# Optimization experiments

Hardware: AMD Instinct MI355X
Metric: run time of the kernel (lower is better)

The kernel has to match this reference:

```python
import jax, jax.numpy as jnp
import numpy as np

N = 262144       # number of samples
DIM = 64         # feature dim
NCLASSES = 128   # number of gaussian classes


def setup_inputs() -> dict:
    key = jax.random.key(0)
    k1, k2, k3, k4 = jax.random.split(key, 4)
    inputs = jax.random.normal(k1, (N, DIM), dtype=jnp.float32)
    target = jax.random.randint(k2, (N,), 0, NCLASSES)
    mean_param = jax.random.normal(k3, (NCLASSES, DIM), dtype=jnp.float32) * 0.02
    cov_param = jax.random.normal(k4, (NCLASSES, DIM, DIM), dtype=jnp.float32) * 0.02
    return {"inputs": inputs, "target": target,
            "mean_param": mean_param, "cov_param": cov_param}


def _l2_distance(sample_mean, sample_cov_sq, mean_param, cov_param):
    # Concrete stand-in for the user-supplied `distance` callable:
    # squared-L2 between the empirical class mean and the learned means,
    # plus the energy of the empirical covariance vector and learned covariances.
    return (jnp.sum((sample_mean[None, :] - mean_param) ** 2)
            + sample_cov_sq
            + jnp.sum(cov_param ** 2))


def reference(inputs, target, mean_param, cov_param):
    nclasses = mean_param.shape[0]
    n = inputs.shape[0]
    # per-class counts and means (fused segmented reduction, one pass)
    counts = jax.ops.segment_sum(jnp.ones((n,), inputs.dtype), target,
                                 num_segments=nclasses)           # [C]
    sums = jax.ops.segment_sum(inputs, target, num_segments=nclasses)  # [C, D]
    means = sums / counts[:, None]                                 # [C, D]
    # center each sample by its class mean  (torch: temp = x - mean)
    temp = inputs - means[target]                                  # [N, D]
    # torch: cov = mm(temp, temp.T).mean(0); row k equals temp_k . mean_j(temp_j)
    # so we only need the per-class sum of centered rows (analytically ~0).
    s = jax.ops.segment_sum(temp, target, num_segments=nclasses)   # [C, D]
    cov = jnp.sum(temp * s[target], axis=-1) / counts[target]      # [N] per-sample entry
    # loss in the python loop is overwritten each iter -> only last class survives
    last = nclasses - 1
    cov_sq_last = jax.ops.segment_sum(cov * cov, target, num_segments=nclasses)[last]
    loss = _l2_distance(means[last], cov_sq_last, mean_param, cov_param)
    return loss
```

## Files before the change

### kernel.cpp

```cpp
#include <hip/hip_runtime.h>


#define DIM 64
#define NCLASSES 128
#define LAST (NCLASSES - 1)
#define NBLOCKS 128
#define BLOCK 512
#define NWAVES (NBLOCKS * 8)
#define SLOT 68
#define COLBASE (NBLOCKS * SLOT)
#define MP_PER_THREAD ((NCLASSES * DIM) / BLOCK)

__global__ __launch_bounds__(BLOCK) void gem_part(
    const float* __restrict__ inputs, const int* __restrict__ target,
    const float* __restrict__ mean_param, const float* __restrict__ cov_param,
    int n, int cov_n4, float* __restrict__ ws)
{
    const int tid  = threadIdx.x;
    const int lane = tid & 63;
    const int wib  = tid >> 6;
    const int b    = blockIdx.x;
    const int gwave = b * 8 + wib;

    const float4* c4 = (const float4*)cov_param;
    const int ci = b * BLOCK + tid;
    float4 v0 = {0.f, 0.f, 0.f, 0.f}, v1 = {0.f, 0.f, 0.f, 0.f};
    if (ci < cov_n4)                  v0 = c4[ci];
    if (ci + NBLOCKS * BLOCK < cov_n4) v1 = c4[ci + NBLOCKS * BLOCK];

    float mp[MP_PER_THREAD];
    if (b == 0) {
        #pragma unroll
        for (int k = 0; k < MP_PER_THREAD; ++k)
            mp[k] = mean_param[tid + k * BLOCK];
    }

    float acc = 0.f;
    int   cnt = 0;
    for (int base = gwave * 256; base < n; base += NWAVES * 256) {
        const int4 t4 = *(const int4*)(target + base + lane * 4);
        unsigned long long m0 = __ballot(t4.x == LAST);
        unsigned long long m1 = __ballot(t4.y == LAST);
        unsigned long long m2 = __ballot(t4.z == LAST);
        unsigned long long m3 = __ballot(t4.w == LAST);
        cnt += __popcll(m0) + __popcll(m1) + __popcll(m2) + __popcll(m3);
        #pragma unroll
        for (int j = 0; j < 4; ++j) {
            unsigned long long m = (j == 0) ? m0 : (j == 1) ? m1 : (j == 2) ? m2 : m3;
            while (m) {
                int bit = __ffsll(m) - 1;
                m &= m - 1;
                acc += inputs[(size_t)(base + 4 * bit + j) * DIM + lane];
            }
        }
    }

    float csum = v0.x * v0.x + v0.y * v0.y + v0.z * v0.z + v0.w * v0.w
               + v1.x * v1.x + v1.y * v1.y + v1.z * v1.z + v1.w * v1.w;
    for (int off = 32; off; off >>= 1) csum += __shfl_down(csum, off, 64);

    float pcol = 0.f, psq = 0.f;
    if (b == 0) {
        #pragma unroll
        for (int k = 0; k < MP_PER_THREAD; ++k) {
            pcol += mp[k];
            psq  += mp[k] * mp[k];
        }
    }
    for (int off = 32; off; off >>= 1) psq += __shfl_down(psq, off, 64);

    __shared__ float sacc[8][DIM];
    __shared__ float scol[8][DIM];
    __shared__ float scov[8], spsq[8];
    __shared__ int   scnt[8];
    sacc[wib][lane] = acc;
    scol[wib][lane] = pcol;
    if (lane == 0) { scov[wib] = csum; scnt[wib] = cnt; spsq[wib] = psq; }
    __syncthreads();

    if (wib == 0) {
        float s = 0.f;
        #pragma unroll
        for (int w = 0; w < 8; ++w) s += sacc[w][lane];
        ws[b * SLOT + lane] = s;
        if (b == 0) {
            float cs = 0.f;
            #pragma unroll
            for (int w = 0; w < 8; ++w) cs += scol[w][lane];
            ws[COLBASE + lane] = cs;
        }
    }
    if (tid == 0) {
        int   c  = 0;   float cv = 0.f, q = 0.f;
        #pragma unroll
        for (int w = 0; w < 8; ++w) { c += scnt[w]; cv += scov[w]; q += spsq[w]; }
        *(float2*)(ws + b * SLOT + DIM) = make_float2((float)c, cv);
        if (b == 0) ws[COLBASE + DIM] = q;
    }
}

__global__ __launch_bounds__(BLOCK) void gem_final(
    const float* __restrict__ ws, float* __restrict__ out)
{
    const int tid  = threadIdx.x;
    const int lane = tid & 63;
    const int g    = tid >> 6;

    const float col = (tid < DIM)  ? ws[COLBASE + tid] : 0.f;
    const float psq = (tid == 0)   ? ws[COLBASE + DIM] : 0.f;

    float s = 0.f;
    #pragma unroll
    for (int j = 0; j < NBLOCKS / 8; ++j)
        s += ws[(g + 8 * j) * SLOT + lane];

    float c = 0.f, cv = 0.f;
    if (tid < NBLOCKS) {
        float2 p = *(const float2*)(ws + tid * SLOT + DIM);
        c = p.x; cv = p.y;
    }
    for (int off = 32; off; off >>= 1) {
        c  += __shfl_down(c,  off, 64);
        cv += __shfl_down(cv, off, 64);
    }

    __shared__ float red[8][DIM];
    __shared__ float scc[2][2];
    __shared__ float spq;
    red[g][lane] = s;
    if (tid < NBLOCKS && lane == 0) { scc[g][0] = c; scc[g][1] = cv; }
    if (tid == 0) spq = psq;
    __syncthreads();

    if (tid < DIM) {
        float tot = 0.f;
        #pragma unroll
        for (int w = 0; w < 8; ++w) tot += red[w][tid];
        const float count = scc[0][0] + scc[1][0];
        const float covs  = scc[0][1] + scc[1][1];
        const float mean  = tot / count;
        float d = (float)NCLASSES * mean * mean - 2.f * mean * col;
        for (int off = 32; off; off >>= 1) d += __shfl_down(d, off, 64);
        if (tid == 0) out[0] = d + covs + spq;
    }
}

extern "C" void kernel_launch(void* const* d_in, const int* in_sizes, int n_in,
                              void* d_out, int out_size, void* d_ws, size_t ws_size,
                              hipStream_t stream) {
    const float* inputs     = (const float*)d_in[0];
    const int*   target     = (const int*)d_in[1];
    const float* mean_param = (const float*)d_in[2];
    const float* cov_param  = (const float*)d_in[3];
    float* out = (float*)d_out;
    float* ws  = (float*)d_ws;

    const int n     = in_sizes[0] / DIM;
    const int cov_n = in_sizes[3];

    gem_part<<<NBLOCKS, BLOCK, 0, stream>>>(inputs, target, mean_param, cov_param,
                                            n, cov_n / 4, ws);
    gem_final<<<1, BLOCK, 0, stream>>>(ws, out);
}
```

Measured before the change: 96.49 us.

## Compact matching sample indices in LDS and balance row gathers across waves

Each block now processes a 2048-sample chunk, compacts the indices of last-class samples into shared memory with a ballot-based prefix scan, and then splits the row gathers evenly across its 8 waves, four independent loads per iteration. Before, each wave serially walked its own ballot mask, so the load was uneven and each row load depended on the previous bit scan. In exchange the loop adds three block-wide barriers per chunk, which may cost more than the imbalance it removes given that only about 1/128 of samples match.

New measurement: 94.61 us. No clear change (-1.9%).

```diff
diff --git a/kernel.cpp b/kernel.cpp
--- a/kernel.cpp
+++ b/kernel.cpp
@@ -7,6 +7,7 @@
 #define NBLOCKS 128
 #define BLOCK 512
 #define NWAVES (NBLOCKS * 8)
+#define CHUNK (BLOCK * 4)
 #define SLOT 68
 #define COLBASE (NBLOCKS * SLOT)
 #define MP_PER_THREAD ((NCLASSES * DIM) / BLOCK)
@@ -20,12 +21,11 @@
     const int lane = tid & 63;
     const int wib  = tid >> 6;
     const int b    = blockIdx.x;
-    const int gwave = b * 8 + wib;
 
     const float4* c4 = (const float4*)cov_param;
     const int ci = b * BLOCK + tid;
     float4 v0 = {0.f, 0.f, 0.f, 0.f}, v1 = {0.f, 0.f, 0.f, 0.f};
-    if (ci < cov_n4)                  v0 = c4[ci];
+    if (ci < cov_n4)                   v0 = c4[ci];
     if (ci + NBLOCKS * BLOCK < cov_n4) v1 = c4[ci + NBLOCKS * BLOCK];
 
     float mp[MP_PER_THREAD];
@@ -35,24 +35,59 @@
             mp[k] = mean_param[tid + k * BLOCK];
     }
 
+    __shared__ int sidx[CHUNK];
+    __shared__ int swcnt[8];
     float acc = 0.f;
-    int   cnt = 0;
-    for (int base = gwave * 256; base < n; base += NWAVES * 256) {
-        const int4 t4 = *(const int4*)(target + base + lane * 4);
-        unsigned long long m0 = __ballot(t4.x == LAST);
-        unsigned long long m1 = __ballot(t4.y == LAST);
-        unsigned long long m2 = __ballot(t4.z == LAST);
-        unsigned long long m3 = __ballot(t4.w == LAST);
-        cnt += __popcll(m0) + __popcll(m1) + __popcll(m2) + __popcll(m3);
+    int   cnt_acc = 0;
+
+    for (int cbase = b * CHUNK; cbase < n; cbase += NBLOCKS * CHUNK) {
+        const int sbase = cbase + wib * 256 + lane * 4;
+        const int4 t4 = *(const int4*)(target + sbase);
+        const unsigned long long m0 = __ballot(t4.x == LAST);
+        const unsigned long long m1 = __ballot(t4.y == LAST);
+        const unsigned long long m2 = __ballot(t4.z == LAST);
+        const unsigned long long m3 = __ballot(t4.w == LAST);
+        const int c0 = __popcll(m0), c1 = __popcll(m1),
+                  c2 = __popcll(m2), c3 = __popcll(m3);
+        if (lane == 0) swcnt[wib] = c0 + c1 + c2 + c3;
+        __syncthreads();
+
+        int woff = 0, tot = 0;
         #pragma unroll
-        for (int j = 0; j < 4; ++j) {
-            unsigned long long m = (j == 0) ? m0 : (j == 1) ? m1 : (j == 2) ? m2 : m3;
-            while (m) {
-                int bit = __ffsll(m) - 1;
-                m &= m - 1;
-                acc += inputs[(size_t)(base + 4 * bit + j) * DIM + lane];
-            }
+        for (int w = 0; w < 8; ++w) {
+            int c = swcnt[w];
+            if (w < wib) woff += c;
+            tot += c;
         }
+
+        const unsigned long long lt = (1ULL << lane) - 1ULL;
+        const int r0 = __popcll(m0 & lt);
+        const int r1 = c0 + __popcll(m1 & lt);
+        const int r2 = c0 + c1 + __popcll(m2 & lt);
+        const int r3 = c0 + c1 + c2 + __popcll(m3 & lt);
+        if (t4.x == LAST) sidx[woff + r0] = sbase + 0;
+        if (t4.y == LAST) sidx[woff + r1] = sbase + 1;
+        if (t4.z == LAST) sidx[woff + r2] = sbase + 2;
+        if (t4.w == LAST) sidx[woff + r3] = sbase + 3;
+        __syncthreads();
+
+        for (int i = wib; i < tot; i += 32) {
+            const int j1 = i + 8, j2 = i + 16, j3 = i + 24;
+            const int s0 = sidx[i];
+            const int s1 = sidx[j1 < tot ? j1 : tot - 1];
+            const int s2 = sidx[j2 < tot ? j2 : tot - 1];
+            const int s3 = sidx[j3 < tot ? j3 : tot - 1];
+            const float x0 = inputs[(size_t)s0 * DIM + lane];
+            const float x1 = inputs[(size_t)s1 * DIM + lane];
+            const float x2 = inputs[(size_t)s2 * DIM + lane];
+            const float x3 = inputs[(size_t)s3 * DIM + lane];
+            acc += x0;
+            if (j1 < tot) acc += x1;
+            if (j2 < tot) acc += x2;
+            if (j3 < tot) acc += x3;
+        }
+        cnt_acc += tot;
+        __syncthreads();
     }
 
     float csum = v0.x * v0.x + v0.y * v0.y + v0.z * v0.z + v0.w * v0.w
@@ -72,10 +107,9 @@
     __shared__ float sacc[8][DIM];
     __shared__ float scol[8][DIM];
     __shared__ float scov[8], spsq[8];
-    __shared__ int   scnt[8];
     sacc[wib][lane] = acc;
     scol[wib][lane] = pcol;
-    if (lane == 0) { scov[wib] = csum; scnt[wib] = cnt; spsq[wib] = psq; }
+    if (lane == 0) { scov[wib] = csum; spsq[wib] = psq; }
     __syncthreads();
 
     if (wib == 0) {
@@ -91,10 +125,10 @@
         }
     }
     if (tid == 0) {
-        int   c  = 0;   float cv = 0.f, q = 0.f;
+        float cv = 0.f, q = 0.f;
         #pragma unroll
-        for (int w = 0; w < 8; ++w) { c += scnt[w]; cv += scov[w]; q += spsq[w]; }
-        *(float2*)(ws + b * SLOT + DIM) = make_float2((float)c, cv);
+        for (int w = 0; w < 8; ++w) { cv += scov[w]; q += spsq[w]; }
+        *(float2*)(ws + b * SLOT + DIM) = make_float2((float)cnt_acc, cv);
         if (b == 0) ws[COLBASE + DIM] = q;
     }
 }
@@ -106,8 +140,8 @@
     const int lane = tid & 63;
     const int g    = tid >> 6;
 
-    const float col = (tid < DIM)  ? ws[COLBASE + tid] : 0.f;
-    const float psq = (tid == 0)   ? ws[COLBASE + DIM] : 0.f;
+    const float col = (tid < DIM) ? ws[COLBASE + tid] : 0.f;
+    const float psq = (tid == 0)  ? ws[COLBASE + DIM] : 0.f;
 
     float s = 0.f;
     #pragma unroll
```
